# Optimization experiments

Measured on AMD Instinct MI355X. Metric: run time of the kernel, lower is better.

The kernel has to match this reference:

```python
import jax, jax.numpy as jnp
import numpy as np

L, B, H, Y, C = 256, 256, 256, 32, 16  # seq len, batch, hidden, y_size, spline channels (u_size+1)


def setup_inputs() -> dict:
    key = jax.random.key(0)
    ks = jax.random.split(key, 10)
    # times: uniform grid 0..L-1 (torchcde default spline parameterization), shape (L,B,1)
    ts = jnp.broadcast_to(jnp.arange(L, dtype=jnp.float32)[:, None, None], (L, B, 1))
    us = jax.random.normal(ks[0], (L, B, C - 1), dtype=jnp.float32)
    h0 = 0.1 * jax.random.normal(ks[1], (B, H), dtype=jnp.float32)
    s = 1.0 / np.sqrt(H)
    # NCDEFunc: Linear(H,H) -> relu -> Linear(H, H*C) -> tanh -> view(B,H,C)
    W1 = jax.random.uniform(ks[2], (H, H), jnp.float32, -s, s)
    b1 = jax.random.uniform(ks[3], (H,), jnp.float32, -s, s)
    W2 = jax.random.uniform(ks[4], (H, H * C), jnp.float32, -s, s)
    b2 = jax.random.uniform(ks[5], (H * C,), jnp.float32, -s, s)
    # decoder MLP(H, 2H, Y, 1): Linear(H,2H) -> tanh -> Linear(2H,Y)
    dW1 = jax.random.uniform(ks[6], (H, 2 * H), jnp.float32, -s, s)
    db1 = jax.random.uniform(ks[7], (2 * H,), jnp.float32, -s, s)
    s2 = 1.0 / np.sqrt(2 * H)
    dW2 = jax.random.uniform(ks[8], (2 * H, Y), jnp.float32, -s2, s2)
    db2 = jax.random.uniform(ks[9], (Y,), jnp.float32, -s2, s2)
    return dict(ts=ts, us=us, h0=h0, W1=W1, b1=b1, W2=W2, b2=b2,
                dW1=dW1, db1=db1, dW2=dW2, db2=db2)


def reference(ts, us, h0, W1, b1, W2, b2, dW1, db1, dW2, db2):
    # permute to batch-first and build control path x: (B, L, C)
    xb = jnp.concatenate([jnp.transpose(ts, (1, 0, 2)), jnp.transpose(us, (1, 0, 2))], axis=2)
    # hermite cubic with backward differences on unit grid (torchcde default t=arange):
    # node derivative d_i = x_i - x_{i-1} (delta=1); d_0 = d_1
    diffs = xb[:, 1:] - xb[:, :-1]                      # (B, L-1, C)
    dnode = jnp.concatenate([diffs[:, :1], diffs], axis=1)  # (B, L, C)
    t = ts[:, 0, 0]  # (L,) -- cdeint t grid = ts.squeeze(-1)[0,:] after permute

    def dXdt(s_):
        # derivative of the hermite cubic spline at scalar time s_ (unit knot spacing)
        idx = jnp.clip(jnp.floor(s_).astype(jnp.int32), 0, L - 2)
        tau = s_ - idx.astype(s_.dtype)
        xi, xip = xb[:, idx], xb[:, idx + 1]            # (B, C)
        di, dip = dnode[:, idx], dnode[:, idx + 1]
        h00p = 6.0 * tau * tau - 6.0 * tau              # h01' = -h00'
        h10p = 3.0 * tau * tau - 4.0 * tau + 1.0
        h11p = 3.0 * tau * tau - 2.0 * tau
        return h00p * (xi - xip) + h10p * di + h11p * dip  # (B, C)

    def vf(z):
        # NCDEFunc: z (B,H) -> matrix (B,H,C)
        hid = jax.nn.relu(z @ W1 + b1)
        return jnp.tanh(hid @ W2 + b2).reshape(B, H, C)

    def step(z, inp):
        s_, dt_ = inp
        dz = jnp.einsum('bhc,bc->bh', vf(z), dXdt(s_))  # f(z) @ dX/dt
        zn = z + dt_ * dz                               # Euler update on grid t
        return zn, zn

    _, zs = jax.lax.scan(step, h0, (t[:-1], t[1:] - t[:-1]))
    z_seq = jnp.concatenate([h0[None], zs], axis=0)     # (L, B, H): cdeint output at all t
    # decoder then permute(1,0,2) -> already time-major here: (L, B, Y)
    return jnp.tanh(z_seq @ dW1 + db1) @ dW2 + db2
```

## Files before the change

### kernel.cpp

```cpp
#include <hip/hip_runtime.h>
#include <math.h>

#define LL 256
#define BB 256
#define HH 256
#define CC 16
#define YY 32
#define HC (HH*CC)
#define NSTEP (LL-1)
#define NBG 32
#define BGB 8
#define HCH 32

__device__ __forceinline__ float ld_coh(const float* p) {
    return __hip_atomic_load(p, __ATOMIC_RELAXED, __HIP_MEMORY_SCOPE_AGENT);
}
__device__ __forceinline__ void st_coh(float* p, float v) {
    __hip_atomic_store(p, v, __ATOMIC_RELAXED, __HIP_MEMORY_SCOPE_AGENT);
}

__device__ __forceinline__ void bg_barrier(unsigned* cnt, unsigned target) {
    __syncthreads();
    if (threadIdx.x == 0) {
        __hip_atomic_fetch_add(cnt, 1u, __ATOMIC_RELAXED, __HIP_MEMORY_SCOPE_AGENT);
        while (__hip_atomic_load(cnt, __ATOMIC_RELAXED, __HIP_MEMORY_SCOPE_AGENT) < target)
            __builtin_amdgcn_s_sleep(8);
    }
    __syncthreads();
}

__global__ void __launch_bounds__(512)
k_scan(const float* __restrict__ us, const float* __restrict__ W1,
       const float* __restrict__ b1, const float* __restrict__ W2,
       const float* __restrict__ b2, float* __restrict__ zs,
       float* __restrict__ hidG, unsigned* __restrict__ barG) {
    __shared__ float z_loc[BGB][HH];
    __shared__ float hidT[HH][BGB];
    __shared__ float pa[BGB][HCH][17];
    __shared__ float psum[4][BGB][512];

    const int bg = blockIdx.x >> 3;
    const int hc = blockIdx.x & 7;
    const int t  = threadIdx.x;
    const int b0 = bg * BGB;
    const int h0 = hc * HCH;
    const int n0 = h0 * CC;

    const int ah  = t & 31;
    const int ajc = t >> 5;
    float w1r[16];
    #pragma unroll
    for (int r = 0; r < 16; r++)
        w1r[r] = W1[(size_t)(ajc * 16 + r) * HH + h0 + ah];

    unsigned* cnt = barG + (size_t)bg * 64;

    const int cg  = t & 127;
    const int jcb = t >> 7;
    const int db  = t >> 6;
    const int hh  = t & 63;
    const int dh  = hh >> 1;
    const int dc0 = (hh & 1) * 8;

    for (int k = 0; k < NSTEP; k++) {
        for (int i = t; i < BGB * HH; i += 512) {
            int b = i >> 8, j = i & 255;
            z_loc[b][j] = ld_coh(&zs[(size_t)k * BB * HH + (size_t)(b0 + b) * HH + j]);
        }
        __syncthreads();

        {
            float acc[BGB];
            #pragma unroll
            for (int b = 0; b < BGB; b++) acc[b] = 0.f;
            #pragma unroll
            for (int r4 = 0; r4 < 4; r4++) {
                #pragma unroll
                for (int b = 0; b < BGB; b++) {
                    float4 zv = *(const float4*)&z_loc[b][ajc * 16 + r4 * 4];
                    acc[b] += zv.x * w1r[r4 * 4 + 0] + zv.y * w1r[r4 * 4 + 1]
                            + zv.z * w1r[r4 * 4 + 2] + zv.w * w1r[r4 * 4 + 3];
                }
            }
            #pragma unroll
            for (int b = 0; b < BGB; b++) pa[b][ah][ajc] = acc[b];
        }
        __syncthreads();
        if (t < 256) {
            int b = t >> 5, h = t & 31;
            float s = b1[h0 + h];
            #pragma unroll
            for (int q = 0; q < 16; q++) s += pa[b][h][q];
            st_coh(&hidG[(size_t)(b0 + b) * HH + h0 + h], fmaxf(s, 0.f));
        }
        bg_barrier(cnt, 8u * (2u * k + 1u));

        for (int i = t; i < BGB * HH; i += 512) {
            int b = i >> 8, j = i & 255;
            hidT[j][b] = ld_coh(&hidG[(size_t)(b0 + b) * HH + j]);
        }
        __syncthreads();

        {
            float acc[BGB][4];
            #pragma unroll
            for (int b = 0; b < BGB; b++)
                #pragma unroll
                for (int q = 0; q < 4; q++) acc[b][q] = 0.f;
            const float* w2p = &W2[(size_t)(jcb * 64) * HC + n0 + cg * 4];
            const int jbase = jcb * 64;
            #pragma unroll 4
            for (int j = 0; j < 64; j++) {
                float4 h03 = *(const float4*)&hidT[jbase + j][0];
                float4 h47 = *(const float4*)&hidT[jbase + j][4];
                float4 w   = *(const float4*)&w2p[(size_t)j * HC];
                acc[0][0] += h03.x * w.x; acc[0][1] += h03.x * w.y;
                acc[0][2] += h03.x * w.z; acc[0][3] += h03.x * w.w;
                acc[1][0] += h03.y * w.x; acc[1][1] += h03.y * w.y;
                acc[1][2] += h03.y * w.z; acc[1][3] += h03.y * w.w;
                acc[2][0] += h03.z * w.x; acc[2][1] += h03.z * w.y;
                acc[2][2] += h03.z * w.z; acc[2][3] += h03.z * w.w;
                acc[3][0] += h03.w * w.x; acc[3][1] += h03.w * w.y;
                acc[3][2] += h03.w * w.z; acc[3][3] += h03.w * w.w;
                acc[4][0] += h47.x * w.x; acc[4][1] += h47.x * w.y;
                acc[4][2] += h47.x * w.z; acc[4][3] += h47.x * w.w;
                acc[5][0] += h47.y * w.x; acc[5][1] += h47.y * w.y;
                acc[5][2] += h47.y * w.z; acc[5][3] += h47.y * w.w;
                acc[6][0] += h47.z * w.x; acc[6][1] += h47.z * w.y;
                acc[6][2] += h47.z * w.z; acc[6][3] += h47.z * w.w;
                acc[7][0] += h47.w * w.x; acc[7][1] += h47.w * w.y;
                acc[7][2] += h47.w * w.z; acc[7][3] += h47.w * w.w;
            }
            #pragma unroll
            for (int b = 0; b < BGB; b++)
                *(float4*)&psum[jcb][b][cg * 4] =
                    make_float4(acc[b][0], acc[b][1], acc[b][2], acc[b][3]);
        }
        __syncthreads();

        {
            float s = 0.f;
            int kk = (k < 1) ? 1 : k;
            const float* usA = &us[((size_t)kk * BB + (b0 + db)) * (CC - 1)];
            const float* usB = &us[((size_t)(kk - 1) * BB + (b0 + db)) * (CC - 1)];
            #pragma unroll
            for (int c = 0; c < 8; c++) {
                int cl  = dc0 + c;
                int col = dh * CC + cl;
                float g = psum[0][db][col] + psum[1][db][col]
                        + psum[2][db][col] + psum[3][db][col] + b2[n0 + col];
                float dval = (cl == 0) ? 1.0f : (usA[cl - 1] - usB[cl - 1]);
                s += tanhf(g) * dval;
            }
            s += __shfl_xor(s, 1);
            if ((hh & 1) == 0) {
                float zn = z_loc[db][h0 + dh] + s;
                st_coh(&zs[(size_t)(k + 1) * BB * HH + (size_t)(b0 + db) * HH + h0 + dh], zn);
            }
        }
        bg_barrier(cnt, 8u * (2u * k + 2u));
    }
}

__global__ void k_out(const float* __restrict__ zseq, const float* __restrict__ dW1,
                      const float* __restrict__ db1, const float* __restrict__ dW2,
                      const float* __restrict__ db2, float* __restrict__ out) {
    __shared__ float zt[16][HH];
    __shared__ float act[16][2 * HH];
    int r0 = blockIdx.x * 16;
    int t  = threadIdx.x;
    {
        const float4* src = (const float4*)(zseq + (size_t)r0 * HH);
        float4* dst = (float4*)&zt[0][0];
        for (int i = t; i < 1024; i += 256) dst[i] = src[i];
    }
    __syncthreads();
    {
        int c0  = (t & 127) * 4;
        int rr0 = (t >> 7) * 8;
        float a[8][4];
        #pragma unroll
        for (int i = 0; i < 8; i++)
            #pragma unroll
            for (int q = 0; q < 4; q++) a[i][q] = 0.f;
        for (int j = 0; j < HH; j++) {
            float4 w = *(const float4*)&dW1[(size_t)j * 2 * HH + c0];
            #pragma unroll
            for (int i = 0; i < 8; i++) {
                float zv = zt[rr0 + i][j];
                a[i][0] += zv * w.x; a[i][1] += zv * w.y;
                a[i][2] += zv * w.z; a[i][3] += zv * w.w;
            }
        }
        float4 bias = *(const float4*)&db1[c0];
        #pragma unroll
        for (int i = 0; i < 8; i++) {
            act[rr0 + i][c0 + 0] = tanhf(a[i][0] + bias.x);
            act[rr0 + i][c0 + 1] = tanhf(a[i][1] + bias.y);
            act[rr0 + i][c0 + 2] = tanhf(a[i][2] + bias.z);
            act[rr0 + i][c0 + 3] = tanhf(a[i][3] + bias.w);
        }
    }
    __syncthreads();
    {
        int rl = t >> 4;
        int y2 = t & 15;
        float o0 = 0.f, o1 = 0.f;
        #pragma unroll 4
        for (int j = 0; j < 2 * HH; j++) {
            float av = act[rl][j];
            float2 w = *(const float2*)&dW2[(size_t)j * YY + y2 * 2];
            o0 += av * w.x; o1 += av * w.y;
        }
        float2 bias = *(const float2*)&db2[y2 * 2];
        out[(size_t)(r0 + rl) * YY + y2 * 2]     = o0 + bias.x;
        out[(size_t)(r0 + rl) * YY + y2 * 2 + 1] = o1 + bias.y;
    }
}

extern "C" void kernel_launch(void* const* d_in, const int* in_sizes, int n_in,
                              void* d_out, int out_size, void* d_ws, size_t ws_size,
                              hipStream_t stream) {
    const float* us  = (const float*)d_in[1];
    const float* h0  = (const float*)d_in[2];
    const float* W1  = (const float*)d_in[3];
    const float* b1  = (const float*)d_in[4];
    const float* W2  = (const float*)d_in[5];
    const float* b2  = (const float*)d_in[6];
    const float* dW1 = (const float*)d_in[7];
    const float* db1 = (const float*)d_in[8];
    const float* dW2 = (const float*)d_in[9];
    const float* db2 = (const float*)d_in[10];
    float* out = (float*)d_out;

    float* zs   = (float*)d_ws;
    float* hidG = zs + (size_t)LL * BB * HH;
    unsigned* barG = (unsigned*)(hidG + (size_t)BB * HH);

    hipMemcpyAsync(zs, h0, (size_t)BB * HH * sizeof(float),
                   hipMemcpyDeviceToDevice, stream);
    hipMemsetAsync(barG, 0, NBG * 64 * sizeof(unsigned), stream);

    k_scan<<<NBG * 8, 512, 0, stream>>>(us, W1, b1, W2, b2, zs, hidG, barG);
    k_out<<<LL * BB / 16, 256, 0, stream>>>(zs, dW1, db1, dW2, db2, out);
}
```

Baseline: 3.963 ms.

## Double threads per block in persistent scan and stage biases and spline derivatives in LDS

Raises the persistent scan kernel from 512 to 1024 threads per block, halving each thread's share of the W1 and W2 work. The second-layer column reduction moves to a per-column layout finished with a 16-lane shuffle. Biases and per-step spline derivative values are cached in shared memory so that global loads of b2 and us no longer repeat inside the inner loop, and the barrier sleep is shortened. The aim is more latency hiding per step on the serial critical path, at the cost of fewer registers per thread and more LDS traffic from the wider reductions.

```diff
diff --git a/kernel.cpp b/kernel.cpp
--- a/kernel.cpp
+++ b/kernel.cpp
@@ -11,6 +11,7 @@
 #define NBG 32
 #define BGB 8
 #define HCH 32
+#define TPB 1024
 
 __device__ __forceinline__ float ld_coh(const float* p) {
     return __hip_atomic_load(p, __ATOMIC_RELAXED, __HIP_MEMORY_SCOPE_AGENT);
@@ -24,20 +25,23 @@
     if (threadIdx.x == 0) {
         __hip_atomic_fetch_add(cnt, 1u, __ATOMIC_RELAXED, __HIP_MEMORY_SCOPE_AGENT);
         while (__hip_atomic_load(cnt, __ATOMIC_RELAXED, __HIP_MEMORY_SCOPE_AGENT) < target)
-            __builtin_amdgcn_s_sleep(8);
-    }
-    __syncthreads();
-}
-
-__global__ void __launch_bounds__(512)
+            __builtin_amdgcn_s_sleep(4);
+    }
+    __syncthreads();
+}
+
+__global__ void __launch_bounds__(TPB)
 k_scan(const float* __restrict__ us, const float* __restrict__ W1,
        const float* __restrict__ b1, const float* __restrict__ W2,
        const float* __restrict__ b2, float* __restrict__ zs,
        float* __restrict__ hidG, unsigned* __restrict__ barG) {
     __shared__ float z_loc[BGB][HH];
     __shared__ float hidT[HH][BGB];
-    __shared__ float pa[BGB][HCH][17];
+    __shared__ float pa[32][BGB * HCH];
     __shared__ float psum[4][BGB][512];
+    __shared__ float b2s[512];
+    __shared__ float dvs[BGB][CC];
+    __shared__ float b1s[HCH];
 
     const int bg = blockIdx.x >> 3;
     const int hc = blockIdx.x & 7;
@@ -46,26 +50,38 @@
     const int h0 = hc * HCH;
     const int n0 = h0 * CC;
 
+    const int ajc = t >> 5;
     const int ah  = t & 31;
-    const int ajc = t >> 5;
-    float w1r[16];
+    float w1r[8];
     #pragma unroll
-    for (int r = 0; r < 16; r++)
-        w1r[r] = W1[(size_t)(ajc * 16 + r) * HH + h0 + ah];
+    for (int r = 0; r < 8; r++)
+        w1r[r] = W1[(size_t)(ajc * 8 + r) * HH + h0 + ah];
+    for (int i = t; i < 512; i += TPB) b2s[i] = b2[n0 + i];
+    if (t < HCH) b1s[t] = b1[h0 + t];
+    __syncthreads();
 
     unsigned* cnt = barG + (size_t)bg * 64;
 
-    const int cg  = t & 127;
-    const int jcb = t >> 7;
-    const int db  = t >> 6;
-    const int hh  = t & 63;
-    const int dh  = hh >> 1;
-    const int dc0 = (hh & 1) * 8;
+    const int jcb = t >> 8;
+    const int cg  = t & 255;
+    const int col = t & 511;
+    const int bh  = (t >> 9) << 2;
 
     for (int k = 0; k < NSTEP; k++) {
-        for (int i = t; i < BGB * HH; i += 512) {
+        const size_t zk = (size_t)k * (BB * HH);
+
+        for (int i = t; i < BGB * HH; i += TPB) {
             int b = i >> 8, j = i & 255;
-            z_loc[b][j] = ld_coh(&zs[(size_t)k * BB * HH + (size_t)(b0 + b) * HH + j]);
+            z_loc[b][j] = ld_coh(&zs[zk + (size_t)(b0 + b) * HH + j]);
+        }
+        if (t < BGB * CC) {
+            int b = t >> 4, c = t & 15;
+            int kk = (k < 1) ? 1 : k;
+            float v = 1.0f;
+            if (c > 0)
+                v = us[((size_t)kk * BB + b0 + b) * (CC - 1) + c - 1]
+                  - us[((size_t)(kk - 1) * BB + b0 + b) * (CC - 1) + c - 1];
+            dvs[b][c] = v;
         }
         __syncthreads();
 
@@ -74,91 +90,79 @@
             #pragma unroll
             for (int b = 0; b < BGB; b++) acc[b] = 0.f;
             #pragma unroll
-            for (int r4 = 0; r4 < 4; r4++) {
+            for (int r2 = 0; r2 < 2; r2++) {
                 #pragma unroll
                 for (int b = 0; b < BGB; b++) {
-                    float4 zv = *(const float4*)&z_loc[b][ajc * 16 + r4 * 4];
-                    acc[b] += zv.x * w1r[r4 * 4 + 0] + zv.y * w1r[r4 * 4 + 1]
-                            + zv.z * w1r[r4 * 4 + 2] + zv.w * w1r[r4 * 4 + 3];
+                    float4 zv = *(const float4*)&z_loc[b][ajc * 8 + r2 * 4];
+                    acc[b] += zv.x * w1r[r2 * 4 + 0] + zv.y * w1r[r2 * 4 + 1]
+                            + zv.z * w1r[r2 * 4 + 2] + zv.w * w1r[r2 * 4 + 3];
                 }
             }
             #pragma unroll
-            for (int b = 0; b < BGB; b++) pa[b][ah][ajc] = acc[b];
-        }
-        __syncthreads();
-        if (t < 256) {
-            int b = t >> 5, h = t & 31;
-            float s = b1[h0 + h];
-            #pragma unroll
-            for (int q = 0; q < 16; q++) s += pa[b][h][q];
-            st_coh(&hidG[(size_t)(b0 + b) * HH + h0 + h], fmaxf(s, 0.f));
-        }
-        bg_barrier(cnt, 8u * (2u * k + 1u));
-
-        for (int i = t; i < BGB * HH; i += 512) {
+            for (int b = 0; b < BGB; b++)
+                pa[ajc][b * HCH + ah] = acc[b];
+        }
+        __syncthreads();
+        if (t < BGB * HCH) {
+            float s = b1s[t & 31];
+            #pragma unroll
+            for (int q = 0; q < 32; q++) s += pa[q][t];
+            st_coh(&hidG[(size_t)(b0 + (t >> 5)) * HH + h0 + (t & 31)],
+                   fmaxf(s, 0.f));
+        }
+        bg_barrier(cnt, 8u * (2u * (unsigned)k + 1u));
+
+        for (int i = t; i < BGB * HH; i += TPB) {
             int b = i >> 8, j = i & 255;
             hidT[j][b] = ld_coh(&hidG[(size_t)(b0 + b) * HH + j]);
         }
         __syncthreads();
 
         {
-            float acc[BGB][4];
-            #pragma unroll
-            for (int b = 0; b < BGB; b++)
-                #pragma unroll
-                for (int q = 0; q < 4; q++) acc[b][q] = 0.f;
-            const float* w2p = &W2[(size_t)(jcb * 64) * HC + n0 + cg * 4];
-            const int jbase = jcb * 64;
+            float a0[BGB], a1[BGB];
+            #pragma unroll
+            for (int b = 0; b < BGB; b++) { a0[b] = 0.f; a1[b] = 0.f; }
+            const float* w2p = &W2[(size_t)(jcb * 64) * HC + n0 + (cg << 1)];
+            const int jb = jcb * 64;
             #pragma unroll 4
             for (int j = 0; j < 64; j++) {
-                float4 h03 = *(const float4*)&hidT[jbase + j][0];
-                float4 h47 = *(const float4*)&hidT[jbase + j][4];
-                float4 w   = *(const float4*)&w2p[(size_t)j * HC];
-                acc[0][0] += h03.x * w.x; acc[0][1] += h03.x * w.y;
-                acc[0][2] += h03.x * w.z; acc[0][3] += h03.x * w.w;
-                acc[1][0] += h03.y * w.x; acc[1][1] += h03.y * w.y;
-                acc[1][2] += h03.y * w.z; acc[1][3] += h03.y * w.w;
-                acc[2][0] += h03.z * w.x; acc[2][1] += h03.z * w.y;
-                acc[2][2] += h03.z * w.z; acc[2][3] += h03.z * w.w;
-                acc[3][0] += h03.w * w.x; acc[3][1] += h03.w * w.y;
-                acc[3][2] += h03.w * w.z; acc[3][3] += h03.w * w.w;
-                acc[4][0] += h47.x * w.x; acc[4][1] += h47.x * w.y;
-                acc[4][2] += h47.x * w.z; acc[4][3] += h47.x * w.w;
-                acc[5][0] += h47.y * w.x; acc[5][1] += h47.y * w.y;
-                acc[5][2] += h47.y * w.z; acc[5][3] += h47.y * w.w;
-                acc[6][0] += h47.z * w.x; acc[6][1] += h47.z * w.y;
-                acc[6][2] += h47.z * w.z; acc[6][3] += h47.z * w.w;
-                acc[7][0] += h47.w * w.x; acc[7][1] += h47.w * w.y;
-                acc[7][2] += h47.w * w.z; acc[7][3] += h47.w * w.w;
+                float4 hA = *(const float4*)&hidT[jb + j][0];
+                float4 hB = *(const float4*)&hidT[jb + j][4];
+                float2 w  = *(const float2*)&w2p[(size_t)j * HC];
+                a0[0] += hA.x * w.x; a1[0] += hA.x * w.y;
+                a0[1] += hA.y * w.x; a1[1] += hA.y * w.y;
+                a0[2] += hA.z * w.x; a1[2] += hA.z * w.y;
+                a0[3] += hA.w * w.x; a1[3] += hA.w * w.y;
+                a0[4] += hB.x * w.x; a1[4] += hB.x * w.y;
+                a0[5] += hB.y * w.x; a1[5] += hB.y * w.y;
+                a0[6] += hB.z * w.x; a1[6] += hB.z * w.y;
+                a0[7] += hB.w * w.x; a1[7] += hB.w * w.y;
             }
             #pragma unroll
             for (int b = 0; b < BGB; b++)
-                *(float4*)&psum[jcb][b][cg * 4] =
-                    make_float4(acc[b][0], acc[b][1], acc[b][2], acc[b][3]);
+                *(float2*)&psum[jcb][b][cg << 1] = make_float2(a0[b], a1[b]);
         }
         __syncthreads();
 
         {
-            float s = 0.f;
-            int kk = (k < 1) ? 1 : k;
-            const float* usA = &us[((size_t)kk * BB + (b0 + db)) * (CC - 1)];
-            const float* usB = &us[((size_t)(kk - 1) * BB + (b0 + db)) * (CC - 1)];
-            #pragma unroll
-            for (int c = 0; c < 8; c++) {
-                int cl  = dc0 + c;
-                int col = dh * CC + cl;
-                float g = psum[0][db][col] + psum[1][db][col]
-                        + psum[2][db][col] + psum[3][db][col] + b2[n0 + col];
-                float dval = (cl == 0) ? 1.0f : (usA[cl - 1] - usB[cl - 1]);
-                s += tanhf(g) * dval;
-            }
-            s += __shfl_xor(s, 1);
-            if ((hh & 1) == 0) {
-                float zn = z_loc[db][h0 + dh] + s;
-                st_coh(&zs[(size_t)(k + 1) * BB * HH + (size_t)(b0 + db) * HH + h0 + dh], zn);
-            }
-        }
-        bg_barrier(cnt, 8u * (2u * k + 2u));
+            #pragma unroll
+            for (int q = 0; q < 4; q++) {
+                int b = bh + q;
+                float g = psum[0][b][col] + psum[1][b][col]
+                        + psum[2][b][col] + psum[3][b][col] + b2s[col];
+                float v = tanhf(g) * dvs[b][col & 15];
+                v += __shfl_xor(v, 1);
+                v += __shfl_xor(v, 2);
+                v += __shfl_xor(v, 4);
+                v += __shfl_xor(v, 8);
+                if ((col & 15) == 0) {
+                    int hl = col >> 4;
+                    st_coh(&zs[zk + (size_t)(BB * HH) + (size_t)(b0 + b) * HH + h0 + hl],
+                           z_loc[b][h0 + hl] + v);
+                }
+            }
+        }
+        bg_barrier(cnt, 8u * (2u * (unsigned)k + 2u));
     }
 }
 
@@ -241,6 +245,6 @@
                    hipMemcpyDeviceToDevice, stream);
     hipMemsetAsync(barG, 0, NBG * 64 * sizeof(unsigned), stream);
 
-    k_scan<<<NBG * 8, 512, 0, stream>>>(us, W1, b1, W2, b2, zs, hidG, barG);
+    k_scan<<<NBG * 8, TPB, 0, stream>>>(us, W1, b1, W2, b2, zs, hidG, barG);
     k_out<<<LL * BB / 16, 256, 0, stream>>>(zs, dW1, db1, dW2, db2, out);
 }
```

After: 3.852 ms. 2.8% less time.
